# Kernel optimization log

Measured on AMD Instinct MI355X. Metric: run time of the kernel, lower is better.

The kernel has to match this reference:

```python
import jax, jax.numpy as jnp
import numpy as np

NUM_POINTS = 128  # num_points from __init__
INF = 1e10       # matches torch.ones * 1e10 init


def setup_inputs() -> dict:
    key = jax.random.key(0)
    k1, k2 = jax.random.split(key)
    B, T, N, C = 4, 16, 8192, 64
    features = jax.random.normal(k1, (B, T, N, C), dtype=jnp.float32)
    farthest_init = jax.random.randint(k2, (B,), 0, T * N, dtype=jnp.int32)
    return {"features": features, "farthest_init": farthest_init}


def reference(features, farthest_init):
    B = features.shape[0]
    C = features.shape[-1]
    points = features.reshape(B, -1, C)          # (B, N, C), N = T*H*W or T*N
    N = points.shape[1]

    def step(carry, _):
        distance, farthest = carry               # (B, N), (B,)
        # gather current centroid: (B, 1, C)
        centroid = jnp.take_along_axis(points, farthest[:, None, None], axis=1)
        dist = jnp.sum((points - centroid) ** 2, axis=2)   # (B, N)
        # masked update distance[mask] = dist[mask] == elementwise min
        distance = jnp.minimum(distance, dist)
        new_farthest = jnp.argmax(distance, axis=1).astype(jnp.int32)
        return (distance, new_farthest), farthest

    init = (jnp.full((B, N), INF, dtype=points.dtype), farthest_init.astype(jnp.int32))
    _, centroids = jax.lax.scan(step, init, None, length=NUM_POINTS)
    centroids = centroids.T                       # (B, NUM_POINTS)

    # gather sampled features: (B, NUM_POINTS, C)
    sampled = jnp.take_along_axis(points, centroids[:, :, None], axis=1)
    return sampled, centroids
```

## Files before the change

### kernel.cpp

```cpp
#include <hip/hip_runtime.h>
#include <stdint.h>


#define NB 4
#define NPTS 131072
#define NC 64
#define NK 128
#define BPB 256
#define NT 256
#define STRIDE (BPB * NT)

__device__ __forceinline__ void amax2(float& bd, int& bi, float od, int oi) {
  if (od > bd || (od == bd && oi < bi)) { bd = od; bi = oi; }
}

__device__ __forceinline__ float dist_np(const float4* __restrict__ p4,
                                         const float4* __restrict__ c4) {
#pragma clang fp contract(off)
  float r0, r1, r2, r3, r4, r5, r6, r7;
  {
    float4 a = p4[0], b = c4[0];
    float dx = a.x - b.x, dy = a.y - b.y, dz = a.z - b.z, dw = a.w - b.w;
    r0 = dx * dx; r1 = dy * dy; r2 = dz * dz; r3 = dw * dw;
    a = p4[1]; b = c4[1];
    dx = a.x - b.x; dy = a.y - b.y; dz = a.z - b.z; dw = a.w - b.w;
    r4 = dx * dx; r5 = dy * dy; r6 = dz * dz; r7 = dw * dw;
  }
#pragma unroll
  for (int blk = 1; blk < 8; ++blk) {
    float4 a = p4[2 * blk], b = c4[2 * blk];
    float dx = a.x - b.x, dy = a.y - b.y, dz = a.z - b.z, dw = a.w - b.w;
    r0 += dx * dx; r1 += dy * dy; r2 += dz * dz; r3 += dw * dw;
    a = p4[2 * blk + 1]; b = c4[2 * blk + 1];
    dx = a.x - b.x; dy = a.y - b.y; dz = a.z - b.z; dw = a.w - b.w;
    r4 += dx * dx; r5 += dy * dy; r6 += dz * dz; r7 += dw * dw;
  }
  return ((r0 + r1) + (r2 + r3)) + ((r4 + r5) + (r6 + r7));
}

__global__ __launch_bounds__(NT, 4) void fps_kernel(
    const float* __restrict__ points,
    const int* __restrict__ finit,
    float* __restrict__ out,
    unsigned long long* __restrict__ slots,
    unsigned long long* __restrict__ fbc) {
  const int x   = blockIdx.x & 7;
  const int q   = blockIdx.x >> 3;
  const int bt  = x >> 1;
  const int ck  = (q << 1) | (x & 1);
  const int tid = threadIdx.x;

  __shared__ float cent[NC];
  __shared__ float red_d[NT / 64];
  __shared__ int   red_i[NT / 64];
  __shared__ int   f_sh;
  __shared__ int   hist[NK];

  const float* __restrict__ P = points + (size_t)bt * NPTS * NC;
  unsigned long long* S = slots + bt * BPB;

  int f = finit[bt];
  if (ck == 0 && tid == 0) hist[0] = f;

  const int i0 = ck * NT + tid;
  const int i1 = i0 + STRIDE;
  float dloc0 = 1e10f, dloc1 = 1e10f;

  for (int k = 0; k < NK - 1; ++k) {
    if (tid < NC / 4) {
      ((float4*)cent)[tid] = ((const float4*)(P + (size_t)f * NC))[tid];
    }
    __syncthreads();

    float bd = -1.0f; int bi = 0;
    {
      const float d = dist_np((const float4*)(P + (size_t)i0 * NC),
                              (const float4*)cent);
      dloc0 = fminf(dloc0, d);
      if (dloc0 > bd) { bd = dloc0; bi = i0; }
    }
    {
      const float d = dist_np((const float4*)(P + (size_t)i1 * NC),
                              (const float4*)cent);
      dloc1 = fminf(dloc1, d);
      if (dloc1 > bd) { bd = dloc1; bi = i1; }
    }

    #pragma unroll
    for (int off = 32; off > 0; off >>= 1) {
      const float od = __shfl_down(bd, off);
      const int   oi = __shfl_down(bi, off);
      amax2(bd, bi, od, oi);
    }
    if ((tid & 63) == 0) { red_d[tid >> 6] = bd; red_i[tid >> 6] = bi; }
    __syncthreads();

    const unsigned tag = (unsigned)(k + 1);

    if (tid == 0) {
      #pragma unroll
      for (int w = 1; w < NT / 64; ++w) amax2(bd, bi, red_d[w], red_i[w]);
      const unsigned long long pack =
          ((unsigned long long)__float_as_uint(bd) << 32) |
          ((unsigned long long)(tag & 0xffu) << 24) |
          (unsigned long long)(unsigned)bi;
      __hip_atomic_store(&S[ck], pack, __ATOMIC_RELAXED,
                         __HIP_MEMORY_SCOPE_AGENT);
    }

    if (ck == 0) {
      if (tid < 64) {
        float pd = -1.0f; int pi = 0;
        #pragma unroll
        for (int s = 0; s < BPB / 64; ++s) {
          const int sl = tid + s * 64;
          unsigned long long v;
          for (;;) {
            v = __hip_atomic_load(&S[sl], __ATOMIC_RELAXED,
                                  __HIP_MEMORY_SCOPE_AGENT);
            if (((unsigned)(v >> 24) & 0xffu) == tag) break;
            __builtin_amdgcn_s_sleep(1);
          }
          amax2(pd, pi, __uint_as_float((unsigned)(v >> 32)),
                (int)(v & 0xffffffu));
        }
        #pragma unroll
        for (int off = 32; off > 0; off >>= 1) {
          const float od = __shfl_down(pd, off);
          const int   oi = __shfl_down(pi, off);
          amax2(pd, pi, od, oi);
        }
        if (tid == 0) {
          f_sh = pi;
          hist[k + 1] = pi;
          const unsigned long long fp =
              ((unsigned long long)(tag & 0xffu) << 24) |
              (unsigned long long)(unsigned)pi;
          __hip_atomic_store(&fbc[bt], fp, __ATOMIC_RELAXED,
                             __HIP_MEMORY_SCOPE_AGENT);
        }
      }
    } else {
      if (tid == 0) {
        unsigned long long v;
        for (;;) {
          v = __hip_atomic_load(&fbc[bt], __ATOMIC_RELAXED,
                                __HIP_MEMORY_SCOPE_AGENT);
          if (((unsigned)(v >> 24) & 0xffu) == tag) break;
          __builtin_amdgcn_s_sleep(1);
        }
        f_sh = (int)(v & 0xffffffu);
      }
    }
    __syncthreads();
    f = f_sh;
  }

  if (ck == 0) {
    for (int e = tid; e < NK; e += NT) {
      out[NB * NK * NC + bt * NK + e] = (float)hist[e];
    }
    for (int e = tid; e < NK * NC; e += NT) {
      const int kk = e >> 6, c = e & (NC - 1);
      out[((size_t)bt * NK + kk) * NC + c] = P[(size_t)hist[kk] * NC + c];
    }
  }
}

extern "C" void kernel_launch(void* const* d_in, const int* in_sizes, int n_in,
                              void* d_out, int out_size, void* d_ws,
                              size_t ws_size, hipStream_t stream) {
  const float* points = (const float*)d_in[0];
  const int* finit = (const int*)d_in[1];
  float* out = (float*)d_out;
  unsigned long long* slots = (unsigned long long*)d_ws;
  unsigned long long* fbc =
      (unsigned long long*)((char*)d_ws + (size_t)NB * BPB * 8);

  void* args[] = {&points, &finit, &out, &slots, &fbc};
  hipError_t err = hipLaunchCooperativeKernel(
      (void*)fps_kernel, dim3(NB * BPB), dim3(NT), args, 0, stream);
  if (err != hipSuccess) {
    fps_kernel<<<dim3(NB * BPB), dim3(NT), 0, stream>>>(points, finit, out,
                                                        slots, fbc);
  }
}
```

Baseline: 2.641 ms.

## Transpose per-block points into coalesced workspace layout before FPS iterations

Each block first copies its two points per thread into a workspace buffer laid out feature-chunk-major, so that in every iteration a wavefront's float4 loads are contiguous across lanes instead of strided by 256 bytes. This targets the uncoalesced global loads repeated over 127 iterations. The block-to-batch mapping also changes from interleaved to contiguous. It costs an extra 128 MB workspace write plus read up front, and it only takes effect if the workspace is large enough.

```diff
diff --git a/kernel.cpp b/kernel.cpp
--- a/kernel.cpp
+++ b/kernel.cpp
@@ -5,33 +5,37 @@
 #define NB 4
 #define NPTS 131072
 #define NC 64
+#define NC4 16
 #define NK 128
 #define BPB 256
 #define NT 256
 #define STRIDE (BPB * NT)
+#define TBLK 8192
+#define T_OFF 65536
 
 __device__ __forceinline__ void amax2(float& bd, int& bi, float od, int oi) {
   if (od > bd || (od == bd && oi < bi)) { bd = od; bi = oi; }
 }
 
-__device__ __forceinline__ float dist_np(const float4* __restrict__ p4,
-                                         const float4* __restrict__ c4) {
+template <int S>
+__device__ __forceinline__ float dist_np_s(const float4* __restrict__ p4,
+                                           const float4* __restrict__ c4) {
 #pragma clang fp contract(off)
   float r0, r1, r2, r3, r4, r5, r6, r7;
   {
     float4 a = p4[0], b = c4[0];
     float dx = a.x - b.x, dy = a.y - b.y, dz = a.z - b.z, dw = a.w - b.w;
     r0 = dx * dx; r1 = dy * dy; r2 = dz * dz; r3 = dw * dw;
-    a = p4[1]; b = c4[1];
+    a = p4[S]; b = c4[1];
     dx = a.x - b.x; dy = a.y - b.y; dz = a.z - b.z; dw = a.w - b.w;
     r4 = dx * dx; r5 = dy * dy; r6 = dz * dz; r7 = dw * dw;
   }
 #pragma unroll
   for (int blk = 1; blk < 8; ++blk) {
-    float4 a = p4[2 * blk], b = c4[2 * blk];
+    float4 a = p4[(2 * blk) * S], b = c4[2 * blk];
     float dx = a.x - b.x, dy = a.y - b.y, dz = a.z - b.z, dw = a.w - b.w;
     r0 += dx * dx; r1 += dy * dy; r2 += dz * dz; r3 += dw * dw;
-    a = p4[2 * blk + 1]; b = c4[2 * blk + 1];
+    a = p4[(2 * blk + 1) * S]; b = c4[2 * blk + 1];
     dx = a.x - b.x; dy = a.y - b.y; dz = a.z - b.z; dw = a.w - b.w;
     r4 += dx * dx; r5 += dy * dy; r6 += dz * dz; r7 += dw * dw;
   }
@@ -43,11 +47,10 @@
     const int* __restrict__ finit,
     float* __restrict__ out,
     unsigned long long* __restrict__ slots,
-    unsigned long long* __restrict__ fbc) {
-  const int x   = blockIdx.x & 7;
-  const int q   = blockIdx.x >> 3;
-  const int bt  = x >> 1;
-  const int ck  = (q << 1) | (x & 1);
+    unsigned long long* __restrict__ fbc,
+    float4* __restrict__ tb) {
+  const int bt  = blockIdx.x >> 8;
+  const int ck  = blockIdx.x & (BPB - 1);
   const int tid = threadIdx.x;
 
   __shared__ float cent[NC];
@@ -59,30 +62,56 @@
   const float* __restrict__ P = points + (size_t)bt * NPTS * NC;
   unsigned long long* S = slots + bt * BPB;
 
+  const int i0 = ck * NT + tid;
+  const int i1 = i0 + STRIDE;
+  const int w = tid >> 6, lane = tid & 63;
+
+  float4* tb_blk = tb ? tb + (size_t)blockIdx.x * TBLK : nullptr;
+  const float4* b0 = nullptr;
+  const float4* b1 = nullptr;
+  if (tb) {
+    {
+      const float4* src = (const float4*)(P + (size_t)i0 * NC);
+      float4* dst = tb_blk + (size_t)((0 * 4 + w) * NC4) * 64 + lane;
+      #pragma unroll
+      for (int c = 0; c < NC4; ++c) dst[c * 64] = src[c];
+      b0 = dst;
+    }
+    {
+      const float4* src = (const float4*)(P + (size_t)i1 * NC);
+      float4* dst = tb_blk + (size_t)((1 * 4 + w) * NC4) * 64 + lane;
+      #pragma unroll
+      for (int c = 0; c < NC4; ++c) dst[c * 64] = src[c];
+      b1 = dst;
+    }
+  }
+
   int f = finit[bt];
   if (ck == 0 && tid == 0) hist[0] = f;
 
-  const int i0 = ck * NT + tid;
-  const int i1 = i0 + STRIDE;
   float dloc0 = 1e10f, dloc1 = 1e10f;
 
   for (int k = 0; k < NK - 1; ++k) {
-    if (tid < NC / 4) {
+    if (tid < NC4) {
       ((float4*)cent)[tid] = ((const float4*)(P + (size_t)f * NC))[tid];
     }
     __syncthreads();
 
     float bd = -1.0f; int bi = 0;
-    {
-      const float d = dist_np((const float4*)(P + (size_t)i0 * NC),
-                              (const float4*)cent);
-      dloc0 = fminf(dloc0, d);
+    const float4* c4 = (const float4*)cent;
+    if (tb) {
+      const float d0 = dist_np_s<64>(b0, c4);
+      dloc0 = fminf(dloc0, d0);
       if (dloc0 > bd) { bd = dloc0; bi = i0; }
-    }
-    {
-      const float d = dist_np((const float4*)(P + (size_t)i1 * NC),
-                              (const float4*)cent);
-      dloc1 = fminf(dloc1, d);
+      const float d1 = dist_np_s<64>(b1, c4);
+      dloc1 = fminf(dloc1, d1);
+      if (dloc1 > bd) { bd = dloc1; bi = i1; }
+    } else {
+      const float d0 = dist_np_s<1>((const float4*)(P + (size_t)i0 * NC), c4);
+      dloc0 = fminf(dloc0, d0);
+      if (dloc0 > bd) { bd = dloc0; bi = i0; }
+      const float d1 = dist_np_s<1>((const float4*)(P + (size_t)i1 * NC), c4);
+      dloc1 = fminf(dloc1, d1);
       if (dloc1 > bd) { bd = dloc1; bi = i1; }
     }
 
@@ -99,7 +128,7 @@
 
     if (tid == 0) {
       #pragma unroll
-      for (int w = 1; w < NT / 64; ++w) amax2(bd, bi, red_d[w], red_i[w]);
+      for (int ww = 1; ww < NT / 64; ++ww) amax2(bd, bi, red_d[ww], red_i[ww]);
       const unsigned long long pack =
           ((unsigned long long)__float_as_uint(bd) << 32) |
           ((unsigned long long)(tag & 0xffu) << 24) |
@@ -177,11 +206,17 @@
   unsigned long long* fbc =
       (unsigned long long*)((char*)d_ws + (size_t)NB * BPB * 8);
 
-  void* args[] = {&points, &finit, &out, &slots, &fbc};
+  const size_t t_bytes = (size_t)NB * BPB * TBLK * sizeof(float4);
+  float4* tb = nullptr;
+  if (ws_size >= (size_t)T_OFF + t_bytes) {
+    tb = (float4*)((char*)d_ws + T_OFF);
+  }
+
+  void* args[] = {&points, &finit, &out, &slots, &fbc, &tb};
   hipError_t err = hipLaunchCooperativeKernel(
       (void*)fps_kernel, dim3(NB * BPB), dim3(NT), args, 0, stream);
   if (err != hipSuccess) {
     fps_kernel<<<dim3(NB * BPB), dim3(NT), 0, stream>>>(points, finit, out,
-                                                        slots, fbc);
-  }
-}
+                                                        slots, fbc, tb);
+  }
+}
```

After: 3.136 ms. 1.19x slower.
